# Kernel tuning notes

Measured on AMD Instinct MI355X. Metric: run time of the kernel, lower is better.

## Reference

```python
import jax, jax.numpy as jnp
import numpy as np
import math

N_HEAD = 16
EPS = 1e-6


def _phi(x, omega):
    # x: (B, nh, T, d), omega: (d, m) -> (B, nh, T, m)
    m = omega.shape[1]
    proj = jnp.einsum('bhtd,dm->bhtm', x, omega)
    norm_sq_half = 0.5 * jnp.sum(x * x, axis=-1, keepdims=True)
    return jnp.exp(proj - norm_sq_half) / math.sqrt(m)


def setup_inputs() -> dict:
    key = jax.random.key(0)
    ks = jax.random.split(key, 4)
    B, T, C = 2, 1024, 1024
    d_h, m = C // N_HEAD, 128
    x = jax.random.normal(ks[0], (B, T, C), dtype=jnp.float32)
    W_attn = jax.random.normal(ks[1], (C, 3 * C), dtype=jnp.float32) * (1.0 / math.sqrt(C))
    b_attn = jnp.zeros((3 * C,), dtype=jnp.float32)
    W_proj = jax.random.normal(ks[2], (C, C), dtype=jnp.float32) * (1.0 / math.sqrt(C))
    b_proj = jnp.zeros((C,), dtype=jnp.float32)
    omega = jax.random.normal(ks[3], (d_h, m), dtype=jnp.float32)
    return {"x": x, "W_attn": W_attn, "b_attn": b_attn, "W_proj": W_proj, "b_proj": b_proj, "omega": omega}


def reference(x, W_attn, b_attn, W_proj, b_proj, omega):
    B, T, C = x.shape
    nh = N_HEAD
    d_h = C // nh
    # fused QKV projection
    qkv = x @ W_attn + b_attn  # (B, T, 3C)
    q, k, v = jnp.split(qkv, 3, axis=-1)
    # (B, nh, T, d_h)
    q = q.reshape(B, T, nh, d_h).transpose(0, 2, 1, 3)
    k = k.reshape(B, T, nh, d_h).transpose(0, 2, 1, 3)
    v = v.reshape(B, T, nh, d_h).transpose(0, 2, 1, 3)
    scale = 1.0 / math.sqrt(d_h)
    q = q * scale
    k = k * scale
    phi_q = _phi(q, omega)  # (B, nh, T, m)
    phi_k = _phi(k, omega)  # (B, nh, T, m)
    # outer-product state: kv (B, nh, T, m, d_h), causal prefix sums
    kv = phi_k[..., :, None] * v[..., None, :]
    S = jnp.cumsum(kv, axis=2)          # (B, nh, T, m, d_h)
    Z = jnp.cumsum(phi_k, axis=2)       # (B, nh, T, m)
    num = jnp.einsum('bhtm,bhtmd->bhtd', phi_q, S)
    den = jnp.einsum('bhtm,bhtm->bht', phi_q, Z)[..., None] + EPS
    y = num / den                       # (B, nh, T, d_h)
    y = y.transpose(0, 2, 1, 3).reshape(B, T, C)
    return y @ W_proj + b_proj
```

## Files before the change

kernel.cpp:

```cpp
#include <hip/hip_runtime.h>
#include <math.h>

#define B_ 2
#define T_ 1024
#define C_ 1024
#define NH 16
#define DH 64
#define M_ 128
#define LCH 64
#define NC (T_/LCH)
#define DEXT 80

constexpr float SCALE = 0.125f;
constexpr float EPSV = 1e-6f;
constexpr float INV_SQRT_M = 0.088388347648318447f;

typedef _Float16 f16;
typedef f16 f16x4 __attribute__((ext_vector_type(4)));
typedef f16 f16x8 __attribute__((ext_vector_type(8)));
typedef float f32x4 __attribute__((ext_vector_type(4)));

typedef const __attribute__((address_space(1))) void* as1_cvoid_p;
typedef __attribute__((address_space(3))) void* as3_void_p;

#define MFMA16 __builtin_amdgcn_mfma_f32_16x16x32_f16

__device__ __forceinline__ void gload16(const void* g, void* l) {
  __builtin_amdgcn_global_load_lds((as1_cvoid_p)g, (as3_void_p)l, 16, 0, 0);
}

__device__ __forceinline__ int sw8(int row, int slot)  { return row * 64  + ((slot ^ (row & 7))  << 3); }
__device__ __forceinline__ int sw16(int row, int slot) { return row * 128 + ((slot ^ (row & 15)) << 3); }

__global__ __launch_bounds__(256) void prep_kernel(const float* __restrict__ x,
                                                   const float* __restrict__ omega,
                                                   const float* __restrict__ Wa,
                                                   const float* __restrict__ Wp,
                                                   f16* __restrict__ x16,
                                                   f16* __restrict__ omT,
                                                   f16* __restrict__ vT,
                                                   f16* __restrict__ B16,
                                                   f16* __restrict__ B16p) {
  __shared__ float tile[32][33];
  int bid = blockIdx.x, tid = threadIdx.x;
  if (bid < 2048) {
    int i = (bid * 256 + tid) * 4;
    float4 v = *(const float4*)&x[i];
    f16x4 o = {(f16)v.x, (f16)v.y, (f16)v.z, (f16)v.w};
    *(f16x4*)&x16[i] = o;
  } else if (bid < 2080) {
    int e = (bid - 2048) * 256 + tid;
    int d = e >> 7, m = e & 127;
    omT[m * 64 + d] = (f16)omega[e];
  } else if (bid < 2592) {
    int idx = bid - 2080;
    int bh = idx >> 4, dr = idx & 15;
    f16 val = (dr == 0) ? (f16)1.0f : (f16)0.0f;
    f16x4 o = {val, val, val, val};
    *(f16x4*)&vT[((size_t)bh * DEXT + 64 + dr) * 1024 + tid * 4] = o;
  } else {
    int tb = bid - 2592;
    const float* in; f16* out; int N, n0, k0;
    if (tb < 3072) { in = Wa; out = B16;  N = 3072; n0 = (tb % 96) * 32; k0 = (tb / 96) * 32; }
    else { tb -= 3072; in = Wp; out = B16p; N = 1024; n0 = (tb & 31) * 32; k0 = (tb >> 5) * 32; }
    int tx = tid & 31, ty = tid >> 5;
    for (int r = ty; r < 32; r += 8)
      tile[r][tx] = in[(size_t)(k0 + r) * N + n0 + tx];
    __syncthreads();
    for (int r = ty; r < 32; r += 8)
      out[(size_t)(n0 + r) * 1024 + k0 + tx] = (f16)tile[tx][r];
  }
}

__global__ __launch_bounds__(256) void gemm_qkv_kernel(
    const f16* __restrict__ A, const f16* __restrict__ B,
    const float* __restrict__ bias, f16* __restrict__ qk16, f16* __restrict__ vT16) {
  __shared__ f16 As[2][128 * 64];
  __shared__ f16 Bs[2][64 * 64];
  const int tid = threadIdx.x;
  const int wid = tid >> 6, lane = tid & 63;
  const int bm = blockIdx.y * 128, bn = blockIdx.x * 64;
  const int wr = (wid >> 1) * 64, wc = (wid & 1) * 32;
  const int srow = lane >> 3, slot = lane & 7;
  const int frow = lane & 15, fkc = lane >> 4;
  f32x4 acc[4][2];
#pragma unroll
  for (int mi = 0; mi < 4; ++mi)
#pragma unroll
    for (int ni = 0; ni < 2; ++ni) acc[mi][ni] = f32x4{0.f, 0.f, 0.f, 0.f};

  auto STAGE = [&](int buf, int kt) {
#pragma unroll
    for (int i = 0; i < 4; ++i) {
      int row = i * 32 + wid * 8 + srow;
      gload16(&A[(size_t)(bm + row) * 1024 + kt + ((slot ^ (row & 7)) << 3)],
              (char*)As[buf] + i * 4096 + wid * 1024);
    }
#pragma unroll
    for (int i = 0; i < 2; ++i) {
      int row = i * 32 + wid * 8 + srow;
      gload16(&B[(size_t)(bn + row) * 1024 + kt + ((slot ^ (row & 7)) << 3)],
              (char*)Bs[buf] + i * 4096 + wid * 1024);
    }
  };
  STAGE(0, 0);
  for (int kt = 0; kt < 1024; kt += 64) {
    const int cur = (kt >> 6) & 1;
    if (kt + 64 < 1024) {
      STAGE(cur ^ 1, kt + 64);
      asm volatile("s_waitcnt vmcnt(6)" ::: "memory");
    } else {
      asm volatile("s_waitcnt vmcnt(0)" ::: "memory");
    }
    __builtin_amdgcn_s_barrier();
    asm volatile("" ::: "memory");
    f16x8 af[4][2], bf[2][2];
#pragma unroll
    for (int mi = 0; mi < 4; ++mi)
#pragma unroll
      for (int kk = 0; kk < 2; ++kk)
        af[mi][kk] = *(const f16x8*)&As[cur][sw8(wr + mi * 16 + frow, kk * 4 + fkc)];
#pragma unroll
    for (int ni = 0; ni < 2; ++ni)
#pragma unroll
      for (int kk = 0; kk < 2; ++kk)
        bf[ni][kk] = *(const f16x8*)&Bs[cur][sw8(wc + ni * 16 + frow, kk * 4 + fkc)];
#pragma unroll
    for (int kk = 0; kk < 2; ++kk)
#pragma unroll
      for (int mi = 0; mi < 4; ++mi)
#pragma unroll
        for (int ni = 0; ni < 2; ++ni)
          acc[mi][ni] = MFMA16(af[mi][kk], bf[ni][kk], acc[mi][ni], 0, 0, 0);
    asm volatile("" ::: "memory");
    __builtin_amdgcn_s_barrier();
  }
#pragma unroll
  for (int ni = 0; ni < 2; ++ni) {
    int col = bn + wc + ni * 16 + frow;
    float bv = bias[col];
#pragma unroll
    for (int mi = 0; mi < 4; ++mi) {
      int row0 = bm + wr + mi * 16 + (lane >> 4) * 4;
#pragma unroll
      for (int r = 0; r < 4; ++r) {
        int row = row0 + r;
        if (col < 2048) {
          qk16[(size_t)row * 2048 + col] = (f16)((acc[mi][ni][r] + bv) * SCALE);
        } else {
          int cc = col - 2048, hh = cc >> 6, d = cc & 63;
          int b = row >> 10, t = row & 1023;
          vT16[((size_t)(b * 16 + hh) * DEXT + d) * 1024 + t] = (f16)(acc[mi][ni][r] + bv);
        }
      }
    }
  }
}

__global__ __launch_bounds__(256) void gemm_out_kernel(
    const f16* __restrict__ A, const f16* __restrict__ B,
    const float* __restrict__ bias, float* __restrict__ C) {
  __shared__ f16 As[2][128 * 64];
  __shared__ f16 Bs[2][64 * 64];
  const int tid = threadIdx.x;
  const int wid = tid >> 6, lane = tid & 63;
  const int bm = blockIdx.y * 128, bn = blockIdx.x * 64;
  const int wr = (wid >> 1) * 64, wc = (wid & 1) * 32;
  const int srow = lane >> 3, slot = lane & 7;
  const int frow = lane & 15, fkc = lane >> 4;
  f32x4 acc[4][2];
#pragma unroll
  for (int mi = 0; mi < 4; ++mi)
#pragma unroll
    for (int ni = 0; ni < 2; ++ni) acc[mi][ni] = f32x4{0.f, 0.f, 0.f, 0.f};

  auto STAGE = [&](int buf, int kt) {
#pragma unroll
    for (int i = 0; i < 4; ++i) {
      int row = i * 32 + wid * 8 + srow;
      gload16(&A[(size_t)(bm + row) * 1024 + kt + ((slot ^ (row & 7)) << 3)],
              (char*)As[buf] + i * 4096 + wid * 1024);
    }
#pragma unroll
    for (int i = 0; i < 2; ++i) {
      int row = i * 32 + wid * 8 + srow;
      gload16(&B[(size_t)(bn + row) * 1024 + kt + ((slot ^ (row & 7)) << 3)],
              (char*)Bs[buf] + i * 4096 + wid * 1024);
    }
  };
  STAGE(0, 0);
  for (int kt = 0; kt < 1024; kt += 64) {
    const int cur = (kt >> 6) & 1;
    if (kt + 64 < 1024) {
      STAGE(cur ^ 1, kt + 64);
      asm volatile("s_waitcnt vmcnt(6)" ::: "memory");
    } else {
      asm volatile("s_waitcnt vmcnt(0)" ::: "memory");
    }
    __builtin_amdgcn_s_barrier();
    asm volatile("" ::: "memory");
    f16x8 af[4][2], bf[2][2];
#pragma unroll
    for (int mi = 0; mi < 4; ++mi)
#pragma unroll
      for (int kk = 0; kk < 2; ++kk)
        af[mi][kk] = *(const f16x8*)&As[cur][sw8(wr + mi * 16 + frow, kk * 4 + fkc)];
#pragma unroll
    for (int ni = 0; ni < 2; ++ni)
#pragma unroll
      for (int kk = 0; kk < 2; ++kk)
        bf[ni][kk] = *(const f16x8*)&Bs[cur][sw8(wc + ni * 16 + frow, kk * 4 + fkc)];
#pragma unroll
    for (int kk = 0; kk < 2; ++kk)
#pragma unroll
      for (int mi = 0; mi < 4; ++mi)
#pragma unroll
        for (int ni = 0; ni < 2; ++ni)
          acc[mi][ni] = MFMA16(af[mi][kk], bf[ni][kk], acc[mi][ni], 0, 0, 0);
    asm volatile("" ::: "memory");
    __builtin_amdgcn_s_barrier();
  }
#pragma unroll
  for (int ni = 0; ni < 2; ++ni) {
    int col = bn + wc + ni * 16 + frow;
    float bv = bias[col];
#pragma unroll
    for (int mi = 0; mi < 4; ++mi) {
      int row0 = bm + wr + mi * 16 + (lane >> 4) * 4;
#pragma unroll
      for (int r = 0; r < 4; ++r)
        C[(size_t)(row0 + r) * 1024 + col] = acc[mi][ni][r] + bv;
    }
  }
}

__global__ __launch_bounds__(256) void chunkS_kernel(const f16* __restrict__ qk16,
                                                     const f16* __restrict__ omT,
                                                     const f16* __restrict__ vT,
                                                     f16* __restrict__ ST) {
  __shared__ f16 om_s[8192];
  __shared__ f16 k_s[4096];
  __shared__ f16 pkT_s[8192];
  __shared__ f16 vt_s[5120];
  __shared__ float nsq_s[64];
  const int tid = threadIdx.x;
  const int wid = tid >> 6, lane = tid & 63;
  const int bc = blockIdx.x;
  const int bh = bc / NC, c = bc % NC;
  const int b = bh >> 4, h = bh & 15;
  const int tbase = c * LCH;
  const int frow = lane & 15, fkc = lane >> 4;
#pragma unroll
  for (int r = 0; r < 4; ++r) {
    int row = r * 32 + wid * 8 + (lane >> 3);
    gload16(omT + row * 64 + ((lane & 7) ^ (row & 7)) * 8,
            (char*)om_s + r * 4096 + wid * 1024);
  }
  {
    int rbase = b * 1024 + tbase, cbase = 1024 + h * 64;
#pragma unroll
    for (int r = 0; r < 2; ++r) {
      int row = r * 32 + wid * 8 + (lane >> 3);
      gload16(qk16 + (size_t)(rbase + row) * 2048 + cbase + ((lane & 7) ^ (row & 7)) * 8,
              (char*)k_s + r * 4096 + wid * 1024);
    }
  }
  for (int rr = wid; rr < 10; rr += 4) {
    int d = rr * 8 + (lane >> 3);
    gload16(vT + ((size_t)bh * DEXT + d) * 1024 + tbase + ((lane & 7) ^ (d & 7)) * 8,
            (char*)vt_s + rr * 1024);
  }
  __syncthreads();
  if (tid < 64) {
    float s = 0.f;
#pragma unroll
    for (int j = 0; j < 8; ++j) {
      f16x8 v = *(const f16x8*)&k_s[sw8(tid, j)];
#pragma unroll
      for (int e = 0; e < 8; ++e) { float f = (float)v[e]; s += f * f; }
    }
    nsq_s[tid] = s;
  }
  f32x4 acc2[8];
#pragma unroll
  for (int cm = 0; cm < 8; ++cm) acc2[cm] = f32x4{0.f, 0.f, 0.f, 0.f};
  {
    f16x8 af2[2], bf2;
#pragma unroll
    for (int kk = 0; kk < 2; ++kk)
      af2[kk] = *(const f16x8*)&k_s[sw8(wid * 16 + frow, kk * 4 + fkc)];
#pragma unroll
    for (int cm = 0; cm < 8; ++cm)
#pragma unroll
      for (int kk = 0; kk < 2; ++kk) {
        bf2 = *(const f16x8*)&om_s[sw8(cm * 16 + frow, kk * 4 + fkc)];
        acc2[cm] = MFMA16(af2[kk], bf2, acc2[cm], 0, 0, 0);
      }
  }
  __syncthreads();
  {
    int t0g = wid * 16 + (lane >> 4) * 4;
    int slot = t0g >> 3, sub = t0g & 4;
    float4 n4 = *(float4*)&nsq_s[t0g];
    float nn[4] = {-0.5f * n4.x, -0.5f * n4.y, -0.5f * n4.z, -0.5f * n4.w};
#pragma unroll
    for (int cm = 0; cm < 8; ++cm) {
      int m = cm * 16 + frow;
      f16x4 o;
#pragma unroll
      for (int r = 0; r < 4; ++r)
        o[r] = (f16)(__expf(acc2[cm][r] + nn[r]) * INV_SQRT_M);
      *(f16x4*)&pkT_s[m * 64 + ((slot ^ (m & 7)) << 3) + sub] = o;
    }
  }
  __syncthreads();
  f32x4 acc[5][2];
#pragma unroll
  for (int dt = 0; dt < 5; ++dt)
#pragma unroll
    for (int cj = 0; cj < 2; ++cj) acc[dt][cj] = f32x4{0.f, 0.f, 0.f, 0.f};
  f16x8 af, bf[2][2];
#pragma unroll
  for (int cj = 0; cj < 2; ++cj)
#pragma unroll
    for (int kk = 0; kk < 2; ++kk)
      bf[cj][kk] = *(const f16x8*)&pkT_s[sw8(wid * 32 + cj * 16 + frow, kk * 4 + fkc)];
#pragma unroll
  for (int dt = 0; dt < 5; ++dt)
#pragma unroll
    for (int kk = 0; kk < 2; ++kk) {
      af = *(const f16x8*)&vt_s[sw8(dt * 16 + frow, kk * 4 + fkc)];
#pragma unroll
      for (int cj = 0; cj < 2; ++cj)
        acc[dt][cj] = MFMA16(af, bf[cj][kk], acc[dt][cj], 0, 0, 0);
    }
  f16* dst = ST + (size_t)bc * (DEXT * 128);
#pragma unroll
  for (int dt = 0; dt < 5; ++dt)
#pragma unroll
    for (int cj = 0; cj < 2; ++cj) {
      int m = wid * 32 + cj * 16 + frow;
      int d0 = dt * 16 + (lane >> 4) * 4;
#pragma unroll
      for (int r = 0; r < 4; ++r)
        dst[(size_t)(d0 + r) * 128 + m] = (f16)acc[dt][cj][r];
    }
}

__global__ __launch_bounds__(256) void prefix_kernel(f16* __restrict__ ST) {
  int tid = threadIdx.x;
  int bh = blockIdx.x;
  int d = blockIdx.y * 16 + (tid >> 4), m0 = (tid & 15) * 8;
  float run[8] = {};
  for (int c = 0; c < NC; ++c) {
    f16* p = ST + ((size_t)(bh * NC + c) * DEXT + d) * 128 + m0;
    f16x8 v = *(f16x8*)p;
    f16x8 o;
#pragma unroll
    for (int j = 0; j < 8; ++j) {
      o[j] = (f16)run[j];
      run[j] += (float)v[j];
    }
    *(f16x8*)p = o;
  }
}

__global__ __launch_bounds__(256) void intra_kernel(const f16* __restrict__ qk16,
    const f16* __restrict__ omT, const f16* __restrict__ vT,
    const f16* __restrict__ ST, f16* __restrict__ y16) {
  __shared__ f16 pq_s[8192];
  __shared__ f16 pk_s[8192];
  __shared__ f16 vt_s[5120];
  __shared__ f16 r2[16384];
  __shared__ float nsq_s[128];
  __shared__ float den_s[64];
  f16* om_s = r2;
  f16* q_s  = r2 + 8192;
  f16* k_s  = r2 + 12288;
  f16* st_s = r2;
  f16* a_s  = r2 + 10240;
  const int tid = threadIdx.x;
  const int wid = tid >> 6, lane = tid & 63;
  const int bc = blockIdx.x;
  const int bh = bc / NC, c = bc % NC;
  const int b = bh >> 4, h = bh & 15;
  const int tbase = c * LCH;
  const int frow = lane & 15, fkc = lane >> 4;
#pragma unroll
  for (int r = 0; r < 4; ++r) {
    int row = r * 32 + wid * 8 + (lane >> 3);
    gload16(omT + row * 64 + ((lane & 7) ^ (row & 7)) * 8,
            (char*)om_s + r * 4096 + wid * 1024);
  }
  {
    int rbase = b * 1024 + tbase;
#pragma unroll
    for (int r = 0; r < 2; ++r) {
      int row = r * 32 + wid * 8 + (lane >> 3);
      int csw = ((lane & 7) ^ (row & 7)) * 8;
      gload16(qk16 + (size_t)(rbase + row) * 2048 + h * 64 + csw,
              (char*)q_s + r * 4096 + wid * 1024);
      gload16(qk16 + (size_t)(rbase + row) * 2048 + 1024 + h * 64 + csw,
              (char*)k_s + r * 4096 + wid * 1024);
    }
  }
  for (int rr = wid; rr < 10; rr += 4) {
    int d = rr * 8 + (lane >> 3);
    gload16(vT + ((size_t)bh * DEXT + d) * 1024 + tbase + ((lane & 7) ^ (d & 7)) * 8,
            (char*)vt_s + rr * 1024);
  }
  __syncthreads();
  if (tid < 128) {
    const f16* src = (tid < 64) ? q_s : k_s;
    int t = tid & 63;
    float s = 0.f;
#pragma unroll
    for (int j = 0; j < 8; ++j) {
      f16x8 v = *(const f16x8*)&src[sw8(t, j)];
#pragma unroll
      for (int e = 0; e < 8; ++e) { float f = (float)v[e]; s += f * f; }
    }
    nsq_s[tid] = s;
  }
  f32x4 acc1q[2][4], acc1k[2][4];
#pragma unroll
  for (int mi = 0; mi < 2; ++mi)
#pragma unroll
    for (int ct = 0; ct < 4; ++ct) {
      acc1q[mi][ct] = f32x4{0.f, 0.f, 0.f, 0.f};
      acc1k[mi][ct] = f32x4{0.f, 0.f, 0.f, 0.f};
    }
  {
    f16x8 af[2][2], bfq, bfk;
#pragma unroll
    for (int mi = 0; mi < 2; ++mi)
#pragma unroll
      for (int kk = 0; kk < 2; ++kk)
        af[mi][kk] = *(const f16x8*)&om_s[sw8(wid * 32 + mi * 16 + frow, kk * 4 + fkc)];
#pragma unroll
    for (int ct = 0; ct < 4; ++ct)
#pragma unroll
      for (int kk = 0; kk < 2; ++kk) {
        bfq = *(const f16x8*)&q_s[sw8(ct * 16 + frow, kk * 4 + fkc)];
        bfk = *(const f16x8*)&k_s[sw8(ct * 16 + frow, kk * 4 + fkc)];
#pragma unroll
        for (int mi = 0; mi < 2; ++mi) {
          acc1q[mi][ct] = MFMA16(af[mi][kk], bfq, acc1q[mi][ct], 0, 0, 0);
          acc1k[mi][ct] = MFMA16(af[mi][kk], bfk, acc1k[mi][ct], 0, 0, 0);
        }
      }
  }
  __syncthreads();
#pragma unroll
  for (int ct = 0; ct < 4; ++ct) {
    int t = ct * 16 + frow;
    float nq = -0.5f * nsq_s[t], nk = -0.5f * nsq_s[64 + t];
#pragma unroll
    for (int mi = 0; mi < 2; ++mi) {
      int m0 = wid * 32 + mi * 16 + (lane >> 4) * 4;
      int addr = t * 128 + (((m0 >> 3) ^ (t & 15)) << 3) + (m0 & 4);
      f16x4 oq, ok;
#pragma unroll
      for (int r = 0; r < 4; ++r) {
        oq[r] = (f16)(__expf(acc1q[mi][ct][r] + nq) * INV_SQRT_M);
        ok[r] = (f16)(__expf(acc1k[mi][ct][r] + nk) * INV_SQRT_M);
      }
      *(f16x4*)&pq_s[addr] = oq;
      *(f16x4*)&pk_s[addr] = ok;
    }
  }
  __syncthreads();
#pragma unroll
  for (int r = 0; r < 5; ++r) {
    int row = r * 16 + wid * 4 + (lane >> 4);
    int col = ((lane & 15) ^ (row & 15)) * 8;
    gload16(ST + (size_t)bc * (DEXT * 128) + (size_t)row * 128 + col,
            (char*)st_s + r * 4096 + wid * 1024);
  }
  {
    f32x4 accq[4];
#pragma unroll
    for (int ct = 0; ct < 4; ++ct) accq[ct] = f32x4{0.f, 0.f, 0.f, 0.f};
    f16x8 af[4], bf;
#pragma unroll
    for (int kk = 0; kk < 4; ++kk)
      af[kk] = *(const f16x8*)&pk_s[sw16(wid * 16 + frow, kk * 4 + fkc)];
#pragma unroll
    for (int ct = 0; ct < 4; ++ct)
#pragma unroll
      for (int kk = 0; kk < 4; ++kk) {
        bf = *(const f16x8*)&pq_s[sw16(ct * 16 + frow, kk * 4 + fkc)];
        accq[ct] = MFMA16(af[kk], bf, accq[ct], 0, 0, 0);
      }
    int tkbase = wid * 16 + fkc * 4;
    int slot = tkbase >> 3, sub = tkbase & 4;
#pragma unroll
    for (int ct = 0; ct < 4; ++ct) {
      int tq = ct * 16 + frow;
      f16x4 av;
#pragma unroll
      for (int r = 0; r < 4; ++r)
        av[r] = (f16)((tkbase + r <= tq) ? accq[ct][r] : 0.f);
      *(f16x4*)&a_s[tq * 64 + ((slot ^ (tq & 7)) << 3) + sub] = av;
    }
  }
  asm volatile("s_waitcnt vmcnt(0)" ::: "memory");
  __syncthreads();
  f32x4 acc2[5];
#pragma unroll
  for (int ct = 0; ct < 5; ++ct) acc2[ct] = f32x4{0.f, 0.f, 0.f, 0.f};
  {
    f16x8 afA[2], afP[4], bfv;
#pragma unroll
    for (int kk = 0; kk < 2; ++kk)
      afA[kk] = *(const f16x8*)&a_s[sw8(wid * 16 + frow, kk * 4 + fkc)];
#pragma unroll
    for (int kk = 0; kk < 4; ++kk)
      afP[kk] = *(const f16x8*)&pq_s[sw16(wid * 16 + frow, kk * 4 + fkc)];
#pragma unroll
    for (int ct = 0; ct < 5; ++ct) {
#pragma unroll
      for (int kk = 0; kk < 2; ++kk) {
        bfv = *(const f16x8*)&vt_s[sw8(ct * 16 + frow, kk * 4 + fkc)];
        acc2[ct] = MFMA16(afA[kk], bfv, acc2[ct], 0, 0, 0);
      }
#pragma unroll
      for (int kk = 0; kk < 4; ++kk) {
        bfv = *(const f16x8*)&st_s[sw16(ct * 16 + frow, kk * 4 + fkc)];
        acc2[ct] = MFMA16(afP[kk], bfv, acc2[ct], 0, 0, 0);
      }
    }
  }
  if (frow == 0) {
    int t0g = wid * 16 + (lane >> 4) * 4;
#pragma unroll
    for (int r = 0; r < 4; ++r) den_s[t0g + r] = acc2[4][r];
  }
  __syncthreads();
  {
    int t0g = wid * 16 + (lane >> 4) * 4;
    float4 d4 = *(float4*)&den_s[t0g];
    float inv[4] = {1.f / (d4.x + EPSV), 1.f / (d4.y + EPSV),
                    1.f / (d4.z + EPSV), 1.f / (d4.w + EPSV)};
#pragma unroll
    for (int ct = 0; ct < 4; ++ct) {
      int d = ct * 16 + frow;
#pragma unroll
      for (int r = 0; r < 4; ++r) {
        int t = t0g + r;
        y16[(size_t)(b * 1024 + tbase + t) * 1024 + h * 64 + d] =
            (f16)(acc2[ct][r] * inv[r]);
      }
    }
  }
}

extern "C" void kernel_launch(void* const* d_in, const int* in_sizes, int n_in,
                              void* d_out, int out_size, void* d_ws, size_t ws_size,
                              hipStream_t stream) {
  const float* x      = (const float*)d_in[0];
  const float* W_attn = (const float*)d_in[1];
  const float* b_attn = (const float*)d_in[2];
  const float* W_proj = (const float*)d_in[3];
  const float* b_proj = (const float*)d_in[4];
  const float* omega  = (const float*)d_in[5];
  float* out = (float*)d_out;

  char* base = (char*)d_ws;
  f16* x16    = (f16*)(base);
  f16* B16    = (f16*)(base + 4194304);
  f16* qk16   = (f16*)(base + 10485760);
  f16* vT16   = (f16*)(base + 18874368);
  f16* ST     = (f16*)(base + 24117248);
  f16* omT16  = (f16*)(base + 34603008);
  f16* B16p   = (f16*)(base + 34619392);
  f16* y16    = (f16*)(base + 36716544);

  prep_kernel<<<6688, 256, 0, stream>>>(x, omega, W_attn, W_proj, x16, omT16, vT16, B16, B16p);
  gemm_qkv_kernel<<<dim3(48, 16), 256, 0, stream>>>(x16, B16, b_attn, qk16, vT16);
  chunkS_kernel<<<512, 256, 0, stream>>>(qk16, omT16, vT16, ST);
  prefix_kernel<<<dim3(32, 5), 256, 0, stream>>>(ST);
  intra_kernel<<<512, 256, 0, stream>>>(qk16, omT16, vT16, ST, y16);
  gemm_out_kernel<<<dim3(16, 16), 256, 0, stream>>>(y16, B16p, b_proj, out);
}
```

Before: 70.63 us.

## Prefetch chunk state early, read omega from global, and use exp2 feature maps

In intra_kernel the chunk-state (ST) loads now go to their own LDS buffer and are issued before the feature-map computation, so their latency overlaps the phi projections instead of being waited on afterwards. Omega is no longer staged through LDS in either chunk kernel; MFMA operands are read directly from global memory (L2-resident). The prep kernel pre-scales omega by log2(e), so the exponentials become a raw v_exp_f32 with the 0.5*|x|^2 term and the 1/sqrt(m) factor folded into an additive constant. This trades a little extra LDS and uncached-latency global operand reads for fewer barriers and less exp arithmetic.

```diff
diff --git a/kernel.cpp b/kernel.cpp
--- a/kernel.cpp
+++ b/kernel.cpp
@@ -13,7 +13,8 @@
 
 constexpr float SCALE = 0.125f;
 constexpr float EPSV = 1e-6f;
-constexpr float INV_SQRT_M = 0.088388347648318447f;
+constexpr float LOG2E = 1.4426950408889634f;
+constexpr float NSQC = -0.72134752044448170f;
 
 typedef _Float16 f16;
 typedef f16 f16x4 __attribute__((ext_vector_type(4)));
@@ -27,6 +28,10 @@
 
 __device__ __forceinline__ void gload16(const void* g, void* l) {
   __builtin_amdgcn_global_load_lds((as1_cvoid_p)g, (as3_void_p)l, 16, 0, 0);
+}
+
+__device__ __forceinline__ float exp2_fast(float x) {
+  float r; asm("v_exp_f32 %0, %1" : "=v"(r) : "v"(x)); return r;
 }
 
 __device__ __forceinline__ int sw8(int row, int slot)  { return row * 64  + ((slot ^ (row & 7))  << 3); }
@@ -51,7 +56,7 @@
   } else if (bid < 2080) {
     int e = (bid - 2048) * 256 + tid;
     int d = e >> 7, m = e & 127;
-    omT[m * 64 + d] = (f16)omega[e];
+    omT[m * 64 + d] = (f16)(omega[e] * LOG2E);
   } else if (bid < 2592) {
     int idx = bid - 2080;
     int bh = idx >> 4, dr = idx & 15;
@@ -238,7 +243,6 @@
                                                      const f16* __restrict__ omT,
                                                      const f16* __restrict__ vT,
                                                      f16* __restrict__ ST) {
-  __shared__ f16 om_s[8192];
   __shared__ f16 k_s[4096];
   __shared__ f16 pkT_s[8192];
   __shared__ f16 vt_s[5120];
@@ -250,12 +254,6 @@
   const int b = bh >> 4, h = bh & 15;
   const int tbase = c * LCH;
   const int frow = lane & 15, fkc = lane >> 4;
-#pragma unroll
-  for (int r = 0; r < 4; ++r) {
-    int row = r * 32 + wid * 8 + (lane >> 3);
-    gload16(omT + row * 64 + ((lane & 7) ^ (row & 7)) * 8,
-            (char*)om_s + r * 4096 + wid * 1024);
-  }
   {
     int rbase = b * 1024 + tbase, cbase = 1024 + h * 64;
 #pragma unroll
@@ -293,7 +291,7 @@
     for (int cm = 0; cm < 8; ++cm)
 #pragma unroll
       for (int kk = 0; kk < 2; ++kk) {
-        bf2 = *(const f16x8*)&om_s[sw8(cm * 16 + frow, kk * 4 + fkc)];
+        bf2 = *(const f16x8*)&omT[(cm * 16 + frow) * 64 + kk * 32 + fkc * 8];
         acc2[cm] = MFMA16(af2[kk], bf2, acc2[cm], 0, 0, 0);
       }
   }
@@ -302,14 +300,15 @@
     int t0g = wid * 16 + (lane >> 4) * 4;
     int slot = t0g >> 3, sub = t0g & 4;
     float4 n4 = *(float4*)&nsq_s[t0g];
-    float nn[4] = {-0.5f * n4.x, -0.5f * n4.y, -0.5f * n4.z, -0.5f * n4.w};
+    float nn[4] = {NSQC * n4.x - 3.5f, NSQC * n4.y - 3.5f,
+                   NSQC * n4.z - 3.5f, NSQC * n4.w - 3.5f};
 #pragma unroll
     for (int cm = 0; cm < 8; ++cm) {
       int m = cm * 16 + frow;
       f16x4 o;
 #pragma unroll
       for (int r = 0; r < 4; ++r)
-        o[r] = (f16)(__expf(acc2[cm][r] + nn[r]) * INV_SQRT_M);
+        o[r] = (f16)exp2_fast(acc2[cm][r] + nn[r]);
       *(f16x4*)&pkT_s[m * 64 + ((slot ^ (m & 7)) << 3) + sub] = o;
     }
   }
@@ -371,14 +370,13 @@
   __shared__ f16 pq_s[8192];
   __shared__ f16 pk_s[8192];
   __shared__ f16 vt_s[5120];
-  __shared__ f16 r2[16384];
+  __shared__ f16 st_s[10240];
+  __shared__ f16 qk2_s[8192];
   __shared__ float nsq_s[128];
   __shared__ float den_s[64];
-  f16* om_s = r2;
-  f16* q_s  = r2 + 8192;
-  f16* k_s  = r2 + 12288;
-  f16* st_s = r2;
-  f16* a_s  = r2 + 10240;
+  f16* q_s = qk2_s;
+  f16* k_s = qk2_s + 4096;
+  f16* a_s = qk2_s;
   const int tid = threadIdx.x;
   const int wid = tid >> 6, lane = tid & 63;
   const int bc = blockIdx.x;
@@ -386,12 +384,6 @@
   const int b = bh >> 4, h = bh & 15;
   const int tbase = c * LCH;
   const int frow = lane & 15, fkc = lane >> 4;
-#pragma unroll
-  for (int r = 0; r < 4; ++r) {
-    int row = r * 32 + wid * 8 + (lane >> 3);
-    gload16(omT + row * 64 + ((lane & 7) ^ (row & 7)) * 8,
-            (char*)om_s + r * 4096 + wid * 1024);
-  }
   {
     int rbase = b * 1024 + tbase;
 #pragma unroll
@@ -409,67 +401,6 @@
     gload16(vT + ((size_t)bh * DEXT + d) * 1024 + tbase + ((lane & 7) ^ (d & 7)) * 8,
             (char*)vt_s + rr * 1024);
   }
-  __syncthreads();
-  if (tid < 128) {
-    const f16* src = (tid < 64) ? q_s : k_s;
-    int t = tid & 63;
-    float s = 0.f;
-#pragma unroll
-    for (int j = 0; j < 8; ++j) {
-      f16x8 v = *(const f16x8*)&src[sw8(t, j)];
-#pragma unroll
-      for (int e = 0; e < 8; ++e) { float f = (float)v[e]; s += f * f; }
-    }
-    nsq_s[tid] = s;
-  }
-  f32x4 acc1q[2][4], acc1k[2][4];
-#pragma unroll
-  for (int mi = 0; mi < 2; ++mi)
-#pragma unroll
-    for (int ct = 0; ct < 4; ++ct) {
-      acc1q[mi][ct] = f32x4{0.f, 0.f, 0.f, 0.f};
-      acc1k[mi][ct] = f32x4{0.f, 0.f, 0.f, 0.f};
-    }
-  {
-    f16x8 af[2][2], bfq, bfk;
-#pragma unroll
-    for (int mi = 0; mi < 2; ++mi)
-#pragma unroll
-      for (int kk = 0; kk < 2; ++kk)
-        af[mi][kk] = *(const f16x8*)&om_s[sw8(wid * 32 + mi * 16 + frow, kk * 4 + fkc)];
-#pragma unroll
-    for (int ct = 0; ct < 4; ++ct)
-#pragma unroll
-      for (int kk = 0; kk < 2; ++kk) {
-        bfq = *(const f16x8*)&q_s[sw8(ct * 16 + frow, kk * 4 + fkc)];
-        bfk = *(const f16x8*)&k_s[sw8(ct * 16 + frow, kk * 4 + fkc)];
-#pragma unroll
-        for (int mi = 0; mi < 2; ++mi) {
-          acc1q[mi][ct] = MFMA16(af[mi][kk], bfq, acc1q[mi][ct], 0, 0, 0);
-          acc1k[mi][ct] = MFMA16(af[mi][kk], bfk, acc1k[mi][ct], 0, 0, 0);
-        }
-      }
-  }
-  __syncthreads();
-#pragma unroll
-  for (int ct = 0; ct < 4; ++ct) {
-    int t = ct * 16 + frow;
-    float nq = -0.5f * nsq_s[t], nk = -0.5f * nsq_s[64 + t];
-#pragma unroll
-    for (int mi = 0; mi < 2; ++mi) {
-      int m0 = wid * 32 + mi * 16 + (lane >> 4) * 4;
-      int addr = t * 128 + (((m0 >> 3) ^ (t & 15)) << 3) + (m0 & 4);
-      f16x4 oq, ok;
-#pragma unroll
-      for (int r = 0; r < 4; ++r) {
-        oq[r] = (f16)(__expf(acc1q[mi][ct][r] + nq) * INV_SQRT_M);
-        ok[r] = (f16)(__expf(acc1k[mi][ct][r] + nk) * INV_SQRT_M);
-      }
-      *(f16x4*)&pq_s[addr] = oq;
-      *(f16x4*)&pk_s[addr] = ok;
-    }
-  }
-  __syncthreads();
 #pragma unroll
   for (int r = 0; r < 5; ++r) {
     int row = r * 16 + wid * 4 + (lane >> 4);
@@ -477,6 +408,67 @@
     gload16(ST + (size_t)bc * (DEXT * 128) + (size_t)row * 128 + col,
             (char*)st_s + r * 4096 + wid * 1024);
   }
+  __syncthreads();
+  if (tid < 128) {
+    const f16* src = (tid < 64) ? q_s : k_s;
+    int t = tid & 63;
+    float s = 0.f;
+#pragma unroll
+    for (int j = 0; j < 8; ++j) {
+      f16x8 v = *(const f16x8*)&src[sw8(t, j)];
+#pragma unroll
+      for (int e = 0; e < 8; ++e) { float f = (float)v[e]; s += f * f; }
+    }
+    nsq_s[tid] = s;
+  }
+  f32x4 acc1q[2][4], acc1k[2][4];
+#pragma unroll
+  for (int mi = 0; mi < 2; ++mi)
+#pragma unroll
+    for (int ct = 0; ct < 4; ++ct) {
+      acc1q[mi][ct] = f32x4{0.f, 0.f, 0.f, 0.f};
+      acc1k[mi][ct] = f32x4{0.f, 0.f, 0.f, 0.f};
+    }
+  {
+    f16x8 af[2][2], bfq, bfk;
+#pragma unroll
+    for (int mi = 0; mi < 2; ++mi)
+#pragma unroll
+      for (int kk = 0; kk < 2; ++kk)
+        af[mi][kk] = *(const f16x8*)&omT[(wid * 32 + mi * 16 + frow) * 64 + kk * 32 + fkc * 8];
+#pragma unroll
+    for (int ct = 0; ct < 4; ++ct)
+#pragma unroll
+      for (int kk = 0; kk < 2; ++kk) {
+        bfq = *(const f16x8*)&q_s[sw8(ct * 16 + frow, kk * 4 + fkc)];
+        bfk = *(const f16x8*)&k_s[sw8(ct * 16 + frow, kk * 4 + fkc)];
+#pragma unroll
+        for (int mi = 0; mi < 2; ++mi) {
+          acc1q[mi][ct] = MFMA16(af[mi][kk], bfq, acc1q[mi][ct], 0, 0, 0);
+          acc1k[mi][ct] = MFMA16(af[mi][kk], bfk, acc1k[mi][ct], 0, 0, 0);
+        }
+      }
+  }
+  __syncthreads();
+#pragma unroll
+  for (int ct = 0; ct < 4; ++ct) {
+    int t = ct * 16 + frow;
+    float nq = NSQC * nsq_s[t] - 3.5f, nk = NSQC * nsq_s[64 + t] - 3.5f;
+#pragma unroll
+    for (int mi = 0; mi < 2; ++mi) {
+      int m0 = wid * 32 + mi * 16 + (lane >> 4) * 4;
+      int addr = t * 128 + (((m0 >> 3) ^ (t & 15)) << 3) + (m0 & 4);
+      f16x4 oq, ok;
+#pragma unroll
+      for (int r = 0; r < 4; ++r) {
+        oq[r] = (f16)exp2_fast(acc1q[mi][ct][r] + nq);
+        ok[r] = (f16)exp2_fast(acc1k[mi][ct][r] + nk);
+      }
+      *(f16x4*)&pq_s[addr] = oq;
+      *(f16x4*)&pk_s[addr] = ok;
+    }
+  }
+  __syncthreads();
   {
     f32x4 accq[4];
 #pragma unroll
@@ -504,7 +496,6 @@
       *(f16x4*)&a_s[tq * 64 + ((slot ^ (tq & 7)) << 3) + sub] = av;
     }
   }
-  asm volatile("s_waitcnt vmcnt(0)" ::: "memory");
   __syncthreads();
   f32x4 acc2[5];
 #pragma unroll
```

Result: slower. 73.43 us (+4.0%).

## Fold the chunk-state prefix sum into intra_kernel and drop prefix_kernel

Applied to the files above, without the earlier changes.

The separate prefix_kernel launch is removed. Each intra_kernel block now sums the chunk states of all earlier chunks in its head straight from global memory into registers, then writes the result into swizzled LDS itself. This removes a kernel launch and a serial 16-step scan over 160 blocks. In exchange it does redundant quadratic reads of ST, roughly half the chunks per block, which should mostly hit cache. The running sum is also kept in fp16 rather than fp32, which loses accuracy.

```diff
diff --git a/kernel.cpp b/kernel.cpp
--- a/kernel.cpp
+++ b/kernel.cpp
@@ -347,24 +347,6 @@
     }
 }
 
-__global__ __launch_bounds__(256) void prefix_kernel(f16* __restrict__ ST) {
-  int tid = threadIdx.x;
-  int bh = blockIdx.x;
-  int d = blockIdx.y * 16 + (tid >> 4), m0 = (tid & 15) * 8;
-  float run[8] = {};
-  for (int c = 0; c < NC; ++c) {
-    f16* p = ST + ((size_t)(bh * NC + c) * DEXT + d) * 128 + m0;
-    f16x8 v = *(f16x8*)p;
-    f16x8 o;
-#pragma unroll
-    for (int j = 0; j < 8; ++j) {
-      o[j] = (f16)run[j];
-      run[j] += (float)v[j];
-    }
-    *(f16x8*)p = o;
-  }
-}
-
 __global__ __launch_bounds__(256) void intra_kernel(const f16* __restrict__ qk16,
     const f16* __restrict__ omT, const f16* __restrict__ vT,
     const f16* __restrict__ ST, f16* __restrict__ y16) {
@@ -409,6 +391,23 @@
     gload16(vT + ((size_t)bh * DEXT + d) * 1024 + tbase + ((lane & 7) ^ (d & 7)) * 8,
             (char*)vt_s + rr * 1024);
   }
+  f16x8 accp[5];
+  {
+    f16x8 z;
+#pragma unroll
+    for (int e = 0; e < 8; ++e) z[e] = (f16)0.f;
+#pragma unroll
+    for (int p = 0; p < 5; ++p) accp[p] = z;
+    const f16* stg = ST + (size_t)(bh * NC) * (DEXT * 128);
+    for (int cp = 0; cp < c; ++cp) {
+      const f16* src = stg + (size_t)cp * (DEXT * 128);
+#pragma unroll
+      for (int p = 0; p < 5; ++p) {
+        f16x8 v = *(const f16x8*)&src[(p * 256 + tid) * 8];
+        accp[p] = accp[p] + v;
+      }
+    }
+  }
   __syncthreads();
   if (tid < 128) {
     const f16* src = (tid < 64) ? q_s : k_s;
@@ -469,14 +468,13 @@
       *(f16x4*)&pk_s[addr] = ok;
     }
   }
-  __syncthreads();
-#pragma unroll
-  for (int r = 0; r < 5; ++r) {
-    int row = r * 16 + wid * 4 + (lane >> 4);
-    int col = ((lane & 15) ^ (row & 15)) * 8;
-    gload16(ST + (size_t)bc * (DEXT * 128) + (size_t)row * 128 + col,
-            (char*)st_s + r * 4096 + wid * 1024);
-  }
+#pragma unroll
+  for (int p = 0; p < 5; ++p) {
+    int j = p * 256 + tid;
+    int row = j >> 4, slot = j & 15;
+    *(f16x8*)&st_s[row * 128 + ((slot ^ (row & 15)) << 3)] = accp[p];
+  }
+  __syncthreads();
   {
     f32x4 accq[4];
 #pragma unroll
@@ -504,7 +502,6 @@
       *(f16x4*)&a_s[tq * 64 + ((slot ^ (tq & 7)) << 3) + sub] = av;
     }
   }
-  asm volatile("s_waitcnt vmcnt(0)" ::: "memory");
   __syncthreads();
   f32x4 acc2[5];
 #pragma unroll
@@ -579,7 +576,6 @@
   prep_kernel<<<6688, 256, 0, stream>>>(x, omega, W_attn, W_proj, x16, omT16, vT16, B16, B16p);
   gemm_qkv_kernel<<<dim3(48, 16), 256, 0, stream>>>(x16, B16, b_attn, qk16, vT16);
   chunkS_kernel<<<512, 256, 0, stream>>>(qk16, omT16, vT16, ST);
-  prefix_kernel<<<dim3(32, 5), 256, 0, stream>>>(ST);
   intra_kernel<<<512, 256, 0, stream>>>(qk16, omT16, vT16, ST, y16);
   gemm_out_kernel<<<dim3(16, 16), 256, 0, stream>>>(y16, B16p, b_proj, out);
 }
```

Measured after the change: 73.28 us. 3.7% more time.

## Fuse chunk prefix scan into chunkS via last-block atomic counter

Applied to the files above, without the earlier changes.

Removes the separate prefix_kernel launch and has the last chunkS block to finish for each (batch, head) run the exclusive prefix sum over all chunk states. A per-head atomic counter, zeroed in prep_kernel, identifies that last block, and thread fences order the writes. This saves a kernel launch and its dependency gap, but the scan now runs in only 32 blocks at the tail of chunkS. The original used 160 blocks, so the tail may become serialized.

```diff
diff --git a/kernel.cpp b/kernel.cpp
--- a/kernel.cpp
+++ b/kernel.cpp
@@ -40,7 +40,8 @@
                                                    f16* __restrict__ omT,
                                                    f16* __restrict__ vT,
                                                    f16* __restrict__ B16,
-                                                   f16* __restrict__ B16p) {
+                                                   f16* __restrict__ B16p,
+                                                   unsigned* __restrict__ cnt) {
   __shared__ float tile[32][33];
   int bid = blockIdx.x, tid = threadIdx.x;
   if (bid < 2048) {
@@ -49,6 +50,7 @@
     f16x4 o = {(f16)v.x, (f16)v.y, (f16)v.z, (f16)v.w};
     *(f16x4*)&x16[i] = o;
   } else if (bid < 2080) {
+    if (bid == 2048 && tid < 32) cnt[tid] = 0u;
     int e = (bid - 2048) * 256 + tid;
     int d = e >> 7, m = e & 127;
     omT[m * 64 + d] = (f16)omega[e];
@@ -237,12 +239,14 @@
 __global__ __launch_bounds__(256) void chunkS_kernel(const f16* __restrict__ qk16,
                                                      const f16* __restrict__ omT,
                                                      const f16* __restrict__ vT,
-                                                     f16* __restrict__ ST) {
+                                                     f16* __restrict__ ST,
+                                                     unsigned* __restrict__ cnt) {
   __shared__ f16 om_s[8192];
   __shared__ f16 k_s[4096];
   __shared__ f16 pkT_s[8192];
   __shared__ f16 vt_s[5120];
   __shared__ float nsq_s[64];
+  __shared__ unsigned lastflag;
   const int tid = threadIdx.x;
   const int wid = tid >> 6, lane = tid & 63;
   const int bc = blockIdx.x;
@@ -345,23 +349,32 @@
       for (int r = 0; r < 4; ++r)
         dst[(size_t)(d0 + r) * 128 + m] = (f16)acc[dt][cj][r];
     }
-}
-
-__global__ __launch_bounds__(256) void prefix_kernel(f16* __restrict__ ST) {
-  int tid = threadIdx.x;
-  int bh = blockIdx.x;
-  int d = blockIdx.y * 16 + (tid >> 4), m0 = (tid & 15) * 8;
-  float run[8] = {};
-  for (int c = 0; c < NC; ++c) {
-    f16* p = ST + ((size_t)(bh * NC + c) * DEXT + d) * 128 + m0;
-    f16x8 v = *(f16x8*)p;
-    f16x8 o;
-#pragma unroll
-    for (int j = 0; j < 8; ++j) {
-      o[j] = (f16)run[j];
-      run[j] += (float)v[j];
-    }
-    *(f16x8*)p = o;
+  __threadfence();
+  if (tid == 0) lastflag = atomicAdd(&cnt[bh], 1u);
+  __syncthreads();
+  if (lastflag == NC - 1) {
+    __threadfence();
+    f16* stg = ST + (size_t)(bh * NC) * (DEXT * 128);
+    float run[5][8];
+#pragma unroll
+    for (int pp = 0; pp < 5; ++pp)
+#pragma unroll
+      for (int j = 0; j < 8; ++j) run[pp][j] = 0.f;
+    for (int cc = 0; cc < NC; ++cc) {
+      f16* p = stg + (size_t)cc * (DEXT * 128);
+#pragma unroll
+      for (int pp = 0; pp < 5; ++pp) {
+        f16* q = &p[(pp * 256 + tid) * 8];
+        f16x8 v = *(f16x8*)q;
+        f16x8 o;
+#pragma unroll
+        for (int j = 0; j < 8; ++j) {
+          o[j] = (f16)run[pp][j];
+          run[pp][j] += (float)v[j];
+        }
+        *(f16x8*)q = o;
+      }
+    }
   }
 }
 
@@ -575,11 +588,11 @@
   f16* omT16  = (f16*)(base + 34603008);
   f16* B16p   = (f16*)(base + 34619392);
   f16* y16    = (f16*)(base + 36716544);
-
-  prep_kernel<<<6688, 256, 0, stream>>>(x, omega, W_attn, W_proj, x16, omT16, vT16, B16, B16p);
+  unsigned* cnt = (unsigned*)(base + 40910848);
+
+  prep_kernel<<<6688, 256, 0, stream>>>(x, omega, W_attn, W_proj, x16, omT16, vT16, B16, B16p, cnt);
   gemm_qkv_kernel<<<dim3(48, 16), 256, 0, stream>>>(x16, B16, b_attn, qk16, vT16);
-  chunkS_kernel<<<512, 256, 0, stream>>>(qk16, omT16, vT16, ST);
-  prefix_kernel<<<dim3(32, 5), 256, 0, stream>>>(ST);
+  chunkS_kernel<<<512, 256, 0, stream>>>(qk16, omT16, vT16, ST, cnt);
   intra_kernel<<<512, 256, 0, stream>>>(qk16, omT16, vT16, ST, y16);
   gemm_out_kernel<<<dim3(16, 16), 256, 0, stream>>>(y16, B16p, b_proj, out);
 }
```

Measured after the change: 150.7 us. +113.3%, slower.
